# Performance work log

Measured on AMD Instinct MI355X. Metric: run time of the kernel, lower is better.

The kernel has to match this reference:

```python
import jax, jax.numpy as jnp
import numpy as np

N = 20000      # nodes
E = 640000     # total atoms across all neighborhoods (edge list length)
CIN = 128
COUT = 128
EPS = 1e-5     # torch BatchNorm1d default eps


def setup_inputs() -> dict:
    key = jax.random.key(0)
    ks = jax.random.split(key, 6)
    x = jax.random.normal(ks[0], (N, CIN), dtype=jnp.float32)
    # neighborhood incidence list: row e says atom src[e] belongs to neighborhood of node tgt[e]
    tgt = jnp.sort(jax.random.randint(ks[1], (E,), 0, N))
    src = jax.random.randint(ks[2], (E,), 0, N)
    # learned params (torch defaults: BN gamma=1, beta=0; Linear weight [out,in])
    gamma1 = jnp.ones((2 * CIN,), jnp.float32)
    beta1 = jnp.zeros((2 * CIN,), jnp.float32)
    W1 = jax.random.normal(ks[3], (CIN, 2 * CIN), jnp.float32) * 0.05
    b1 = jnp.zeros((CIN,), jnp.float32)
    gamma2 = jnp.ones((CIN,), jnp.float32)
    beta2 = jnp.zeros((CIN,), jnp.float32)
    W2 = jax.random.normal(ks[4], (COUT, CIN), jnp.float32) * 0.05
    b2 = jnp.zeros((COUT,), jnp.float32)
    return {"x": x, "gamma1": gamma1, "beta1": beta1, "W1": W1, "b1": b1,
            "gamma2": gamma2, "beta2": beta2, "W2": W2, "b2": b2,
            "tgt": tgt, "src": src}


def _batchnorm(h, gamma, beta):
    # torch BatchNorm1d training-mode forward: normalize with batch mean / biased var
    mu = jnp.mean(h, axis=0)
    var = jnp.var(h, axis=0)  # ddof=0 (biased), matches torch normalization
    return (h - mu) * jax.lax.rsqrt(var + EPS) * gamma + beta


def reference(x, gamma1, beta1, W1, b1, gamma2, beta2, W2, b2, tgt, src):
    n = x.shape[0]
    # transfer1 (ptensors1 singleton domains -> ptensors1 over neighborhoods):
    # per atom row e: [ sum_{i in N(tgt[e])} x[i] , x[src[e]] ]  -> [E, 2*CIN]
    nbr_sum = jax.ops.segment_sum(x[src], tgt, num_segments=n)  # [N, CIN]
    h = jnp.concatenate([nbr_sum[tgt], x[src]], axis=-1)        # [E, 2*CIN]
    h = _batchnorm(h, gamma1, beta1)
    h = jax.nn.relu(h @ W1.T + b1)                              # [E, CIN]
    h = _batchnorm(h, gamma2, beta2)
    h = jax.nn.relu(h @ W2.T + b2)                              # [E, COUT]
    return h  # from_matrix just re-wraps this matrix with the same atoms
```

## Files before the change

### kernel.cpp

```cpp
#include <hip/hip_runtime.h>

#define NN 20000
#define NE 640000
#define Cc 128
#define C2 256
#define BN_EPS 1e-5f

typedef __attribute__((ext_vector_type(8))) short bf16x8;
typedef __attribute__((ext_vector_type(4))) float f32x4;

#define WS_P     0
#define WS_Q     (NN*Cc)
#define WS_CNTT  (2*NN*Cc)
#define WS_CNTS  (2*NN*Cc + NN)
#define WS_STATS (2*NN*Cc + 2*NN)
#define WS_W1PT  (WS_STATS + 768)
#define WS_B1P   (WS_W1PT + C2*Cc)
#define WS_W2BF  (WS_B1P + Cc)
#define WS_B2P   (WS_W2BF + Cc*Cc)


static __device__ inline unsigned short f2bf(float f) {
  union { float f; unsigned u; } v; v.f = f;
  unsigned r = v.u + 0x7fffu + ((v.u >> 16) & 1u);
  return (unsigned short)(r >> 16);
}
static __device__ inline float bf2f(unsigned short h) {
  union { unsigned u; float f; } v; v.u = (unsigned)h << 16; return v.f;
}

__global__ void k_zero(float* __restrict__ stats, int* __restrict__ cntS) {
  int i = blockIdx.x * blockDim.x + threadIdx.x;
  if (i < 768) stats[i] = 0.0f;
  if (i < NN) cntS[i] = 0;
}

__global__ void k_nbr(const float* __restrict__ x, const int* __restrict__ tgt,
                      const int* __restrict__ src, float* __restrict__ nbr,
                      float* __restrict__ cntT, int* __restrict__ cntS) {
  int node = blockIdx.x;
  int a = 0, b = NE;
  while (a < b) { int m = (a + b) >> 1; if (tgt[m] < node) a = m + 1; else b = m; }
  int lo = a;
  b = NE;
  while (a < b) { int m = (a + b) >> 1; if (tgt[m] <= node) a = m + 1; else b = m; }
  int hi = a;
  int c = threadIdx.x;
  for (int e = lo + c; e < hi; e += 128) atomicAdd(&cntS[src[e]], 1);
  float a0 = 0.f, a1 = 0.f, a2 = 0.f, a3 = 0.f;
  int e = lo;
  for (; e + 7 < hi; e += 8) {
    int s0 = src[e],     s1 = src[e + 1], s2 = src[e + 2], s3 = src[e + 3];
    int s4 = src[e + 4], s5 = src[e + 5], s6 = src[e + 6], s7 = src[e + 7];
    float v0 = x[(size_t)s0 * Cc + c], v1 = x[(size_t)s1 * Cc + c];
    float v2 = x[(size_t)s2 * Cc + c], v3 = x[(size_t)s3 * Cc + c];
    float v4 = x[(size_t)s4 * Cc + c], v5 = x[(size_t)s5 * Cc + c];
    float v6 = x[(size_t)s6 * Cc + c], v7 = x[(size_t)s7 * Cc + c];
    a0 += v0 + v4; a1 += v1 + v5; a2 += v2 + v6; a3 += v3 + v7;
  }
  for (; e + 3 < hi; e += 4) {
    int s0 = src[e], s1 = src[e + 1], s2 = src[e + 2], s3 = src[e + 3];
    a0 += x[(size_t)s0 * Cc + c];
    a1 += x[(size_t)s1 * Cc + c];
    a2 += x[(size_t)s2 * Cc + c];
    a3 += x[(size_t)s3 * Cc + c];
  }
  for (; e < hi; ++e) a0 += x[(size_t)src[e] * Cc + c];
  nbr[node * Cc + c] = (a0 + a1) + (a2 + a3);
  if (c == 0) cntT[node] = (float)(hi - lo);
}

__global__ __launch_bounds__(512) void k_stats1(const float* __restrict__ nbr,
                                                const float* __restrict__ x,
                                                const float* __restrict__ cntT,
                                                const int* __restrict__ cntS,
                                                float* __restrict__ stats) {
  __shared__ float ls[3][4][Cc];
  int c = threadIdx.x & 127;
  int y = threadIdx.x >> 7;
  float sa = 0.f, qa = 0.f, sb = 0.f, qb = 0.f;
  for (int t = blockIdx.x + y * 512; t < NN; t += 2048) {
    float ct = cntT[t];
    float cs = (float)cntS[t];
    float v1 = nbr[t * Cc + c];
    float v2 = x[t * Cc + c];
    sa += ct * v1; qa += ct * v1 * v1;
    sb += cs * v2; qb += cs * v2 * v2;
  }
  if (y) {
    ls[y - 1][0][c] = sa; ls[y - 1][1][c] = qa;
    ls[y - 1][2][c] = sb; ls[y - 1][3][c] = qb;
  }
  __syncthreads();
  if (!y) {
    #pragma unroll
    for (int j = 0; j < 3; ++j) {
      sa += ls[j][0][c]; qa += ls[j][1][c];
      sb += ls[j][2][c]; qb += ls[j][3][c];
    }
    atomicAdd(&stats[c], sa);
    atomicAdd(&stats[256 + c], qa);
    atomicAdd(&stats[128 + c], sb);
    atomicAdd(&stats[256 + 128 + c], qb);
  }
}

__global__ void k_fold1(const float* __restrict__ W1, const float* __restrict__ b1,
                        const float* __restrict__ g1, const float* __restrict__ be1,
                        const float* __restrict__ stats,
                        float* __restrict__ W1pT, float* __restrict__ b1p) {
  __shared__ float red[C2];
  int o = blockIdx.x, c = threadIdx.x;
  const float inv = 1.0f / (float)NE;
  float mu = stats[c] * inv;
  float var = stats[256 + c] * inv - mu * mu;
  float a = g1[c] * rsqrtf(var + BN_EPS);
  float cc = be1[c] - mu * a;
  float w = W1[o * C2 + c];
  W1pT[c * Cc + o] = w * a;
  red[c] = w * cc;
  __syncthreads();
  for (int s = 128; s > 0; s >>= 1) { if (c < s) red[c] += red[c + s]; __syncthreads(); }
  if (c == 0) b1p[o] = b1[o] + red[0];
}

__global__ __launch_bounds__(256) void k_pq(const float* __restrict__ nbr,
                                            const float* __restrict__ x,
                                            const float* __restrict__ W1pT,
                                            unsigned short* __restrict__ P,
                                            unsigned short* __restrict__ Q) {
  __shared__ float Ar[32][128];
  const int half = blockIdx.y;
  const float* __restrict__ A = half ? x : nbr;
  unsigned short* __restrict__ Out = half ? Q : P;
  const float* __restrict__ Wt = W1pT + (half ? Cc * Cc : 0);
  int tid = threadIdx.x;
  int r0 = blockIdx.x * 32;
  for (int i = tid; i < 32 * 128; i += 256) {
    int r = i >> 7, c = i & 127;
    Ar[r][c] = A[(r0 + r) * Cc + c];
  }
  __syncthreads();
  int tx = tid & 31, ty = tid >> 5;
  float acc[4][4] = {};
  #pragma unroll 4
  for (int c = 0; c < 128; ++c) {
    float4 w = *(const float4*)&Wt[c * Cc + tx * 4];
    float a0 = Ar[ty * 4 + 0][c], a1 = Ar[ty * 4 + 1][c];
    float a2 = Ar[ty * 4 + 2][c], a3 = Ar[ty * 4 + 3][c];
    acc[0][0] += a0 * w.x; acc[0][1] += a0 * w.y; acc[0][2] += a0 * w.z; acc[0][3] += a0 * w.w;
    acc[1][0] += a1 * w.x; acc[1][1] += a1 * w.y; acc[1][2] += a1 * w.z; acc[1][3] += a1 * w.w;
    acc[2][0] += a2 * w.x; acc[2][1] += a2 * w.y; acc[2][2] += a2 * w.z; acc[2][3] += a2 * w.w;
    acc[3][0] += a3 * w.x; acc[3][1] += a3 * w.y; acc[3][2] += a3 * w.z; acc[3][3] += a3 * w.w;
  }
  #pragma unroll
  for (int i = 0; i < 4; ++i) {
    int node = r0 + ty * 4 + i;
    ushort4 v;
    v.x = f2bf(acc[i][0]); v.y = f2bf(acc[i][1]);
    v.z = f2bf(acc[i][2]); v.w = f2bf(acc[i][3]);
    *(ushort4*)&Out[node * Cc + tx * 4] = v;
  }
}

__global__ __launch_bounds__(512) void k_stats2(const unsigned short* __restrict__ P,
                                                const unsigned short* __restrict__ Q,
                                                const float* __restrict__ b1p,
                                                const int* __restrict__ tgt,
                                                const int* __restrict__ src,
                                                float* __restrict__ stats,
                                                unsigned short* __restrict__ zout) {
  __shared__ float s2[7][Cc], q2[7][Cc];
  const int nwg = NE / 512;
  const int q8 = nwg >> 3, r8 = nwg & 7;
  int orig = blockIdx.x;
  int xcd = orig & 7, idx = orig >> 3;
  int bid = (xcd < r8 ? xcd * (q8 + 1) : r8 * (q8 + 1) + (xcd - r8) * q8) + idx;
  int cp = threadIdx.x & 63;
  int y = threadIdx.x >> 6;
  int c0 = cp * 2;
  int e0 = bid * 512;
  float2 b = *(const float2*)&b1p[c0];
  float s0 = 0.f, s1 = 0.f, q0 = 0.f, q1 = 0.f;
  for (int e = e0 + y * 8; e < e0 + 512; e += 64) {
    int t[8], sr[8];
    #pragma unroll
    for (int j = 0; j < 8; ++j) { t[j] = tgt[e + j]; sr[j] = src[e + j]; }
    ushort2 pv[8], qv[8];
    #pragma unroll
    for (int j = 0; j < 8; ++j) pv[j] = *(const ushort2*)&P[(size_t)t[j] * Cc + c0];
    #pragma unroll
    for (int j = 0; j < 8; ++j) qv[j] = *(const ushort2*)&Q[(size_t)sr[j] * Cc + c0];
    #pragma unroll
    for (int j = 0; j < 8; ++j) {
      float z0 = fmaxf(bf2f(pv[j].x) + bf2f(qv[j].x) + b.x, 0.f);
      float z1 = fmaxf(bf2f(pv[j].y) + bf2f(qv[j].y) + b.y, 0.f);
      ushort2 zz; zz.x = f2bf(z0); zz.y = f2bf(z1);
      *(ushort2*)&zout[(size_t)(e + j) * 256 + c0] = zz;
      s0 += z0; s1 += z1; q0 += z0 * z0; q1 += z1 * z1;
    }
  }
  if (y) { s2[y - 1][c0] = s0; s2[y - 1][c0 + 1] = s1;
           q2[y - 1][c0] = q0; q2[y - 1][c0 + 1] = q1; }
  __syncthreads();
  if (!y) {
    #pragma unroll
    for (int j = 0; j < 7; ++j) {
      s0 += s2[j][c0]; s1 += s2[j][c0 + 1];
      q0 += q2[j][c0]; q1 += q2[j][c0 + 1];
    }
    atomicAdd(&stats[512 + c0], s0);
    atomicAdd(&stats[512 + c0 + 1], s1);
    atomicAdd(&stats[640 + c0], q0);
    atomicAdd(&stats[640 + c0 + 1], q1);
  }
}

__global__ void k_fold2(const float* __restrict__ W2, const float* __restrict__ b2,
                        const float* __restrict__ g2, const float* __restrict__ be2,
                        const float* __restrict__ stats,
                        unsigned short* __restrict__ W2bf, float* __restrict__ b2p) {
  __shared__ float red[Cc];
  int o = blockIdx.x, c = threadIdx.x;
  const float inv = 1.0f / (float)NE;
  float mu = stats[512 + c] * inv;
  float var = stats[640 + c] * inv - mu * mu;
  float a = g2[c] * rsqrtf(var + BN_EPS);
  float cc = be2[c] - mu * a;
  float w = W2[o * Cc + c];
  W2bf[o * Cc + c] = f2bf(w * a);
  red[c] = w * cc;
  __syncthreads();
  for (int s = 64; s > 0; s >>= 1) { if (c < s) red[c] += red[c + s]; __syncthreads(); }
  if (c == 0) b2p[o] = b2[o] + red[0];
}

#define WPAD 136
__global__ __launch_bounds__(256) void k_out_mfma(const unsigned short* __restrict__ zin,
                                                  const unsigned short* __restrict__ W2bf,
                                                  const float* __restrict__ b2p,
                                                  float* __restrict__ out) {
  __shared__ unsigned short Wl[128 * WPAD];
  int tid = threadIdx.x;
  int e0 = blockIdx.x * 64;

  for (int i = tid; i < 2048; i += 256) {
    int row = i >> 4, col = (i & 15) * 8;
    *(bf16x8*)&Wl[row * WPAD + col] = *(const bf16x8*)&W2bf[row * Cc + col];
  }

  int w = tid >> 6, l = tid & 63;
  int la = l & 15, kb = l >> 4;
  int e = e0 + w * 16 + la;

  bf16x8 zfr[4];
  #pragma unroll
  for (int kk = 0; kk < 4; ++kk)
    zfr[kk] = *(const bf16x8*)&zin[(size_t)e * 256 + kk * 32 + kb * 8];
  __syncthreads();

  f32x4 acc[8];
  #pragma unroll
  for (int n = 0; n < 8; ++n) acc[n] = (f32x4){0.f, 0.f, 0.f, 0.f};

  #pragma unroll
  for (int kk = 0; kk < 4; ++kk) {
    #pragma unroll
    for (int n = 0; n < 8; ++n) {
      bf16x8 wa = *(const bf16x8*)&Wl[(n * 16 + la) * WPAD + kk * 32 + kb * 8];
      acc[n] = __builtin_amdgcn_mfma_f32_16x16x32_bf16(wa, zfr[kk], acc[n], 0, 0, 0);
    }
  }

  #pragma unroll
  for (int n = 0; n < 8; ++n) {
    int o0 = n * 16 + kb * 4;
    float4 bb = *(const float4*)&b2p[o0];
    float4 v;
    v.x = fmaxf(acc[n][0] + bb.x, 0.f);
    v.y = fmaxf(acc[n][1] + bb.y, 0.f);
    v.z = fmaxf(acc[n][2] + bb.z, 0.f);
    v.w = fmaxf(acc[n][3] + bb.w, 0.f);
    *(float4*)&out[(size_t)e * Cc + o0] = v;
  }
}

extern "C" void kernel_launch(void* const* d_in, const int* in_sizes, int n_in,
                              void* d_out, int out_size, void* d_ws, size_t ws_size,
                              hipStream_t stream) {
  (void)in_sizes; (void)n_in; (void)out_size; (void)ws_size;
  const float* x   = (const float*)d_in[0];
  const float* g1  = (const float*)d_in[1];
  const float* be1 = (const float*)d_in[2];
  const float* W1  = (const float*)d_in[3];
  const float* b1  = (const float*)d_in[4];
  const float* g2  = (const float*)d_in[5];
  const float* be2 = (const float*)d_in[6];
  const float* W2  = (const float*)d_in[7];
  const float* b2  = (const float*)d_in[8];
  const int* tgt   = (const int*)d_in[9];
  const int* src   = (const int*)d_in[10];

  float* ws  = (float*)d_ws;
  float* out = (float*)d_out;

  unsigned short* P = (unsigned short*)(ws + WS_P);
  unsigned short* Q = (unsigned short*)(ws + WS_Q);
  float* cntT  = ws + WS_CNTT;
  int*   cntS  = (int*)(ws + WS_CNTS);
  float* stats = ws + WS_STATS;
  float* W1pT  = ws + WS_W1PT;
  float* b1p   = ws + WS_B1P;
  unsigned short* W2bf = (unsigned short*)(ws + WS_W2BF);
  float* b2p   = ws + WS_B2P;
  float* nbr   = out;

  k_zero  <<<dim3((NN + 255) / 256), dim3(256), 0, stream>>>(stats, cntS);
  k_nbr   <<<dim3(NN),              dim3(Cc),  0, stream>>>(x, tgt, src, nbr, cntT, cntS);
  k_stats1<<<dim3(512),             dim3(512), 0, stream>>>(nbr, x, cntT, cntS, stats);
  k_fold1 <<<dim3(Cc),              dim3(C2),  0, stream>>>(W1, b1, g1, be1, stats, W1pT, b1p);
  k_pq    <<<dim3(NN / 32, 2),      dim3(256), 0, stream>>>(nbr, x, W1pT, P, Q);
  k_stats2<<<dim3(NE / 512),        dim3(512), 0, stream>>>(P, Q, b1p, tgt, src, stats,
                                                            (unsigned short*)out);
  k_fold2 <<<dim3(Cc),              dim3(Cc),  0, stream>>>(W2, b2, g2, be2, stats, W2bf, b2p);
  k_out_mfma<<<dim3(NE / 64),       dim3(256), 0, stream>>>((const unsigned short*)out,
                                                            W2bf, b2p, out);
}
```

Before: 298.6 us.

## Cast x to bf16 upfront and run node-level first GEMM on MFMA

Adds a kernel that converts x to bf16 once. The neighbor gather, first-layer statistics and node projection then read half as many bytes, and the neighbor sums are stored as bf16. The per-node projection k_pq is rewritten from an fp32 FMA loop to bf16 MFMA 16x16x32 with the folded W1 kept in padded LDS. This lowers gather bandwidth and GEMM time at the cost of bf16 rounding of x and the neighbor sums before the batch statistics, which could affect accuracy.

```diff
diff --git a/kernel.cpp b/kernel.cpp
--- a/kernel.cpp
+++ b/kernel.cpp
@@ -10,12 +10,13 @@
 typedef __attribute__((ext_vector_type(4))) float f32x4;
 
 #define WS_P     0
+#define WS_XBF   (NN*Cc/2)
 #define WS_Q     (NN*Cc)
 #define WS_CNTT  (2*NN*Cc)
 #define WS_CNTS  (2*NN*Cc + NN)
 #define WS_STATS (2*NN*Cc + 2*NN)
-#define WS_W1PT  (WS_STATS + 768)
-#define WS_B1P   (WS_W1PT + C2*Cc)
+#define WS_W1BF  (WS_STATS + 768)
+#define WS_B1P   (WS_W1BF + C2*Cc)
 #define WS_W2BF  (WS_B1P + Cc)
 #define WS_B2P   (WS_W2BF + Cc*Cc)
 
@@ -35,8 +36,21 @@
   if (i < NN) cntS[i] = 0;
 }
 
-__global__ void k_nbr(const float* __restrict__ x, const int* __restrict__ tgt,
-                      const int* __restrict__ src, float* __restrict__ nbr,
+__global__ __launch_bounds__(256) void k_cast(const float* __restrict__ x,
+                                              unsigned short* __restrict__ xbf) {
+  int i = (blockIdx.x * 256 + threadIdx.x) * 8;
+  float4 v0 = *(const float4*)&x[i];
+  float4 v1 = *(const float4*)&x[i + 4];
+  bf16x8 o;
+  o[0] = (short)f2bf(v0.x); o[1] = (short)f2bf(v0.y);
+  o[2] = (short)f2bf(v0.z); o[3] = (short)f2bf(v0.w);
+  o[4] = (short)f2bf(v1.x); o[5] = (short)f2bf(v1.y);
+  o[6] = (short)f2bf(v1.z); o[7] = (short)f2bf(v1.w);
+  *(bf16x8*)&xbf[i] = o;
+}
+
+__global__ void k_nbr(const unsigned short* __restrict__ xbf, const int* __restrict__ tgt,
+                      const int* __restrict__ src, unsigned short* __restrict__ nbr,
                       float* __restrict__ cntT, int* __restrict__ cntS) {
   int node = blockIdx.x;
   int a = 0, b = NE;
@@ -52,26 +66,19 @@
   for (; e + 7 < hi; e += 8) {
     int s0 = src[e],     s1 = src[e + 1], s2 = src[e + 2], s3 = src[e + 3];
     int s4 = src[e + 4], s5 = src[e + 5], s6 = src[e + 6], s7 = src[e + 7];
-    float v0 = x[(size_t)s0 * Cc + c], v1 = x[(size_t)s1 * Cc + c];
-    float v2 = x[(size_t)s2 * Cc + c], v3 = x[(size_t)s3 * Cc + c];
-    float v4 = x[(size_t)s4 * Cc + c], v5 = x[(size_t)s5 * Cc + c];
-    float v6 = x[(size_t)s6 * Cc + c], v7 = x[(size_t)s7 * Cc + c];
+    float v0 = bf2f(xbf[(size_t)s0 * Cc + c]), v1 = bf2f(xbf[(size_t)s1 * Cc + c]);
+    float v2 = bf2f(xbf[(size_t)s2 * Cc + c]), v3 = bf2f(xbf[(size_t)s3 * Cc + c]);
+    float v4 = bf2f(xbf[(size_t)s4 * Cc + c]), v5 = bf2f(xbf[(size_t)s5 * Cc + c]);
+    float v6 = bf2f(xbf[(size_t)s6 * Cc + c]), v7 = bf2f(xbf[(size_t)s7 * Cc + c]);
     a0 += v0 + v4; a1 += v1 + v5; a2 += v2 + v6; a3 += v3 + v7;
   }
-  for (; e + 3 < hi; e += 4) {
-    int s0 = src[e], s1 = src[e + 1], s2 = src[e + 2], s3 = src[e + 3];
-    a0 += x[(size_t)s0 * Cc + c];
-    a1 += x[(size_t)s1 * Cc + c];
-    a2 += x[(size_t)s2 * Cc + c];
-    a3 += x[(size_t)s3 * Cc + c];
-  }
-  for (; e < hi; ++e) a0 += x[(size_t)src[e] * Cc + c];
-  nbr[node * Cc + c] = (a0 + a1) + (a2 + a3);
+  for (; e < hi; ++e) a0 += bf2f(xbf[(size_t)src[e] * Cc + c]);
+  nbr[(size_t)node * Cc + c] = f2bf((a0 + a1) + (a2 + a3));
   if (c == 0) cntT[node] = (float)(hi - lo);
 }
 
-__global__ __launch_bounds__(512) void k_stats1(const float* __restrict__ nbr,
-                                                const float* __restrict__ x,
+__global__ __launch_bounds__(512) void k_stats1(const unsigned short* __restrict__ nbr,
+                                                const unsigned short* __restrict__ xbf,
                                                 const float* __restrict__ cntT,
                                                 const int* __restrict__ cntS,
                                                 float* __restrict__ stats) {
@@ -82,8 +89,8 @@
   for (int t = blockIdx.x + y * 512; t < NN; t += 2048) {
     float ct = cntT[t];
     float cs = (float)cntS[t];
-    float v1 = nbr[t * Cc + c];
-    float v2 = x[t * Cc + c];
+    float v1 = bf2f(nbr[(size_t)t * Cc + c]);
+    float v2 = bf2f(xbf[(size_t)t * Cc + c]);
     sa += ct * v1; qa += ct * v1 * v1;
     sb += cs * v2; qb += cs * v2 * v2;
   }
@@ -108,7 +115,7 @@
 __global__ void k_fold1(const float* __restrict__ W1, const float* __restrict__ b1,
                         const float* __restrict__ g1, const float* __restrict__ be1,
                         const float* __restrict__ stats,
-                        float* __restrict__ W1pT, float* __restrict__ b1p) {
+                        unsigned short* __restrict__ W1bf, float* __restrict__ b1p) {
   __shared__ float red[C2];
   int o = blockIdx.x, c = threadIdx.x;
   const float inv = 1.0f / (float)NE;
@@ -117,49 +124,65 @@
   float a = g1[c] * rsqrtf(var + BN_EPS);
   float cc = be1[c] - mu * a;
   float w = W1[o * C2 + c];
-  W1pT[c * Cc + o] = w * a;
+  W1bf[(size_t)(c >> 7) * Cc * Cc + o * Cc + (c & 127)] = f2bf(w * a);
   red[c] = w * cc;
   __syncthreads();
   for (int s = 128; s > 0; s >>= 1) { if (c < s) red[c] += red[c + s]; __syncthreads(); }
   if (c == 0) b1p[o] = b1[o] + red[0];
 }
 
-__global__ __launch_bounds__(256) void k_pq(const float* __restrict__ nbr,
-                                            const float* __restrict__ x,
-                                            const float* __restrict__ W1pT,
+#define WPAD 136
+__global__ __launch_bounds__(256) void k_pq(const unsigned short* __restrict__ nbr,
+                                            const unsigned short* __restrict__ xbf,
+                                            const unsigned short* __restrict__ W1bf,
                                             unsigned short* __restrict__ P,
                                             unsigned short* __restrict__ Q) {
-  __shared__ float Ar[32][128];
+  __shared__ unsigned short Wl[128 * WPAD];
   const int half = blockIdx.y;
-  const float* __restrict__ A = half ? x : nbr;
+  const unsigned short* __restrict__ A = half ? xbf : nbr;
   unsigned short* __restrict__ Out = half ? Q : P;
-  const float* __restrict__ Wt = W1pT + (half ? Cc * Cc : 0);
+  const unsigned short* __restrict__ Wt = W1bf + (size_t)half * Cc * Cc;
   int tid = threadIdx.x;
-  int r0 = blockIdx.x * 32;
-  for (int i = tid; i < 32 * 128; i += 256) {
-    int r = i >> 7, c = i & 127;
-    Ar[r][c] = A[(r0 + r) * Cc + c];
-  }
-  __syncthreads();
-  int tx = tid & 31, ty = tid >> 5;
-  float acc[4][4] = {};
-  #pragma unroll 4
-  for (int c = 0; c < 128; ++c) {
-    float4 w = *(const float4*)&Wt[c * Cc + tx * 4];
-    float a0 = Ar[ty * 4 + 0][c], a1 = Ar[ty * 4 + 1][c];
-    float a2 = Ar[ty * 4 + 2][c], a3 = Ar[ty * 4 + 3][c];
-    acc[0][0] += a0 * w.x; acc[0][1] += a0 * w.y; acc[0][2] += a0 * w.z; acc[0][3] += a0 * w.w;
-    acc[1][0] += a1 * w.x; acc[1][1] += a1 * w.y; acc[1][2] += a1 * w.z; acc[1][3] += a1 * w.w;
-    acc[2][0] += a2 * w.x; acc[2][1] += a2 * w.y; acc[2][2] += a2 * w.z; acc[2][3] += a2 * w.w;
-    acc[3][0] += a3 * w.x; acc[3][1] += a3 * w.y; acc[3][2] += a3 * w.z; acc[3][3] += a3 * w.w;
-  }
-  #pragma unroll
-  for (int i = 0; i < 4; ++i) {
-    int node = r0 + ty * 4 + i;
-    ushort4 v;
-    v.x = f2bf(acc[i][0]); v.y = f2bf(acc[i][1]);
-    v.z = f2bf(acc[i][2]); v.w = f2bf(acc[i][3]);
-    *(ushort4*)&Out[node * Cc + tx * 4] = v;
+  int n0 = blockIdx.x * 64;
+
+  for (int i = tid; i < 2048; i += 256) {
+    int row = i >> 4, col = (i & 15) * 8;
+    *(bf16x8*)&Wl[row * WPAD + col] = *(const bf16x8*)&Wt[row * Cc + col];
+  }
+
+  int w = tid >> 6, l = tid & 63;
+  int la = l & 15, kb = l >> 4;
+  int node = n0 + w * 16 + la;
+  int ld = node < NN ? node : NN - 1;
+
+  bf16x8 zfr[4];
+  #pragma unroll
+  for (int kk = 0; kk < 4; ++kk)
+    zfr[kk] = *(const bf16x8*)&A[(size_t)ld * Cc + kk * 32 + kb * 8];
+  __syncthreads();
+
+  f32x4 acc[8];
+  #pragma unroll
+  for (int n = 0; n < 8; ++n) acc[n] = (f32x4){0.f, 0.f, 0.f, 0.f};
+
+  #pragma unroll
+  for (int kk = 0; kk < 4; ++kk) {
+    #pragma unroll
+    for (int n = 0; n < 8; ++n) {
+      bf16x8 wa = *(const bf16x8*)&Wl[(n * 16 + la) * WPAD + kk * 32 + kb * 8];
+      acc[n] = __builtin_amdgcn_mfma_f32_16x16x32_bf16(wa, zfr[kk], acc[n], 0, 0, 0);
+    }
+  }
+
+  if (node < NN) {
+    #pragma unroll
+    for (int n = 0; n < 8; ++n) {
+      int o0 = n * 16 + kb * 4;
+      ushort4 v;
+      v.x = f2bf(acc[n][0]); v.y = f2bf(acc[n][1]);
+      v.z = f2bf(acc[n][2]); v.w = f2bf(acc[n][3]);
+      *(ushort4*)&Out[(size_t)node * Cc + o0] = v;
+    }
   }
 }
 
@@ -235,7 +258,6 @@
   if (c == 0) b2p[o] = b2[o] + red[0];
 }
 
-#define WPAD 136
 __global__ __launch_bounds__(256) void k_out_mfma(const unsigned short* __restrict__ zin,
                                                   const unsigned short* __restrict__ W2bf,
                                                   const float* __restrict__ b2p,
@@ -304,22 +326,24 @@
   float* ws  = (float*)d_ws;
   float* out = (float*)d_out;
 
-  unsigned short* P = (unsigned short*)(ws + WS_P);
-  unsigned short* Q = (unsigned short*)(ws + WS_Q);
+  unsigned short* P    = (unsigned short*)(ws + WS_P);
+  unsigned short* xbf  = (unsigned short*)(ws + WS_XBF);
+  unsigned short* Q    = (unsigned short*)(ws + WS_Q);
   float* cntT  = ws + WS_CNTT;
   int*   cntS  = (int*)(ws + WS_CNTS);
   float* stats = ws + WS_STATS;
-  float* W1pT  = ws + WS_W1PT;
+  unsigned short* W1bf = (unsigned short*)(ws + WS_W1BF);
   float* b1p   = ws + WS_B1P;
   unsigned short* W2bf = (unsigned short*)(ws + WS_W2BF);
   float* b2p   = ws + WS_B2P;
-  float* nbr   = out;
+  unsigned short* nbr  = (unsigned short*)out;
 
   k_zero  <<<dim3((NN + 255) / 256), dim3(256), 0, stream>>>(stats, cntS);
-  k_nbr   <<<dim3(NN),              dim3(Cc),  0, stream>>>(x, tgt, src, nbr, cntT, cntS);
-  k_stats1<<<dim3(512),             dim3(512), 0, stream>>>(nbr, x, cntT, cntS, stats);
-  k_fold1 <<<dim3(Cc),              dim3(C2),  0, stream>>>(W1, b1, g1, be1, stats, W1pT, b1p);
-  k_pq    <<<dim3(NN / 32, 2),      dim3(256), 0, stream>>>(nbr, x, W1pT, P, Q);
+  k_cast  <<<dim3(NN * Cc / 2048),   dim3(256), 0, stream>>>(x, xbf);
+  k_nbr   <<<dim3(NN),              dim3(Cc),  0, stream>>>(xbf, tgt, src, nbr, cntT, cntS);
+  k_stats1<<<dim3(512),             dim3(512), 0, stream>>>(nbr, xbf, cntT, cntS, stats);
+  k_fold1 <<<dim3(Cc),              dim3(C2),  0, stream>>>(W1, b1, g1, be1, stats, W1bf, b1p);
+  k_pq    <<<dim3((NN + 63) / 64, 2), dim3(256), 0, stream>>>(nbr, xbf, W1bf, P, Q);
   k_stats2<<<dim3(NE / 512),        dim3(512), 0, stream>>>(P, Q, b1p, tgt, src, stats,
                                                             (unsigned short*)out);
   k_fold2 <<<dim3(Cc),              dim3(Cc),  0, stream>>>(W2, b2, g2, be2, stats, W2bf, b2p);
```

Result: faster. 281.0 us (-5.9%).
